# Kernel tuning notes

Hardware: AMD Instinct MI355X
Metric: run time of the kernel (lower is better)

Reference implementation:

```python
import jax, jax.numpy as jnp
import numpy as np

N_NODES = 50000
N_EDGES = 800000
IN_CH = 256
H1, D1 = 4, 64   # layer 1: 4 heads x 64 -> 256
H2, D2 = 1, 64   # output layer: 1 head x 64
NEG_SLOPE = 0.2  # DGL GATConv default


def _leaky_relu(x):
    return jnp.where(x >= 0, x, NEG_SLOPE * x)


def gat_conv(h, src, dst, W, attn_l, attn_r, bias, res_W, num_heads, out_feats, apply_elu):
    """DGL GATConv (eval mode, feat_drop=attn_drop=0).
    h: (N, F_in); src/dst: (E,) edge endpoints (edge u->v aggregates at v).
    W: (F_in, H*D); attn_l/attn_r: (H, D); bias: (H*D,); res_W: (F_in, H*D) or None.
    Returns (N, H, D).
    """
    N = h.shape[0]
    ft = (h @ W).reshape(N, num_heads, out_feats)            # (N,H,D)
    el = jnp.sum(ft * attn_l, axis=-1)                        # (N,H)
    er = jnp.sum(ft * attn_r, axis=-1)                        # (N,H)
    e = _leaky_relu(el[src] + er[dst])                        # (E,H)
    # segment softmax over incoming edges of each dst node
    emax = jax.ops.segment_max(e, dst, num_segments=N)        # (N,H)
    emax = jax.lax.stop_gradient(emax)
    ee = jnp.exp(e - emax[dst])                               # (E,H)
    denom = jax.ops.segment_sum(ee, dst, num_segments=N)      # (N,H)
    a = ee / denom[dst]                                       # (E,H)
    msg = ft[src] * a[:, :, None]                             # (E,H,D)
    rst = jax.ops.segment_sum(msg, dst, num_segments=N)       # (N,H,D)
    if res_W is not None:
        rst = rst + (h @ res_W).reshape(N, num_heads, out_feats)
    rst = rst + bias.reshape(num_heads, out_feats)
    if apply_elu:
        rst = jax.nn.elu(rst)
    return rst


def setup_inputs() -> dict:
    key = jax.random.key(0)
    ks = jax.random.split(key, 12)
    feat = jax.random.normal(ks[0], (N_NODES, IN_CH), dtype=jnp.float32)
    src = jax.random.randint(ks[1], (N_EDGES,), 0, N_NODES)
    dst = jax.random.randint(ks[2], (N_EDGES,), 0, N_NODES)
    s = 0.1
    W1 = jax.random.normal(ks[3], (IN_CH, H1 * D1), dtype=jnp.float32) * s
    al1 = jax.random.normal(ks[4], (H1, D1), dtype=jnp.float32) * s
    ar1 = jax.random.normal(ks[5], (H1, D1), dtype=jnp.float32) * s
    b1 = jnp.zeros((H1 * D1,), dtype=jnp.float32)
    W2 = jax.random.normal(ks[6], (H1 * D1, H2 * D2), dtype=jnp.float32) * s
    al2 = jax.random.normal(ks[7], (H2, D2), dtype=jnp.float32) * s
    ar2 = jax.random.normal(ks[8], (H2, D2), dtype=jnp.float32) * s
    b2 = jnp.zeros((H2 * D2,), dtype=jnp.float32)
    resW2 = jax.random.normal(ks[9], (H1 * D1, H2 * D2), dtype=jnp.float32) * s
    return {"feat": feat, "src": src, "dst": dst,
            "W1": W1, "al1": al1, "ar1": ar1, "b1": b1,
            "W2": W2, "al2": al2, "ar2": ar2, "b2": b2, "resW2": resW2}


def reference(feat, src, dst, W1, al1, ar1, b1, W2, al2, ar2, b2, resW2):
    # Layer 1: 4 heads, ELU, no residual (first DGL layer built without residual)
    h = gat_conv(feat, src, dst, W1, al1, ar1, b1, None, H1, D1, True)
    h = h.reshape(N_NODES, H1 * D1)  # flatten(1)
    # Layer 2: 1 head, residual (linear res_fc since 256 != 64), no activation
    h = gat_conv(h, src, dst, W2, al2, ar2, b2, resW2, H2, D2, False)
    return h.mean(axis=1)  # mean over output heads -> (N, out_channels)
```

## Files before the change

### kernel.cpp

```cpp
#include <hip/hip_runtime.h>
#include <math.h>

#define N_NODES 50000
#define N_EDGES 800000
#define ELL_W 64

#define NB 98
#define BCAP 10240
#define BIN_BLKS 250
#define CONV_BLKS 256

typedef __attribute__((ext_vector_type(8))) short bf16x8;
typedef __attribute__((ext_vector_type(4))) float f32x4;
typedef __attribute__((ext_vector_type(2))) float f32x2;

__device__ __forceinline__ float leaky(float x) { return x >= 0.f ? x : 0.2f * x; }
__device__ __forceinline__ unsigned short f2bf(float f) {
  unsigned u = __float_as_uint(f);
  return (unsigned short)((u + 0x7fffu + ((u >> 16) & 1u)) >> 16);
}
__device__ __forceinline__ float bflo(unsigned u) { return __uint_as_float(u << 16); }
__device__ __forceinline__ float bfhi(unsigned u) { return __uint_as_float(u & 0xffff0000u); }
__device__ __forceinline__ unsigned pack2(float a, float b) {
  return (unsigned)f2bf(a) | ((unsigned)f2bf(b) << 16);
}
__device__ __forceinline__ unsigned pack2u(unsigned a, unsigned b) {
  return pack2(__uint_as_float(a), __uint_as_float(b));
}

__launch_bounds__(256)
__global__ void prep_k(const float* __restrict__ W1, const float* __restrict__ W2,
                       const float* __restrict__ resW2, short* __restrict__ Wt1,
                       short* __restrict__ Wt2, const int* __restrict__ src,
                       const int* __restrict__ dst, unsigned* __restrict__ gcnt,
                       unsigned* __restrict__ bbuf) {
  __shared__ int hist[NB];
  __shared__ int basev[NB];
  if (blockIdx.x < BIN_BLKS) {
    const int e0 = blockIdx.x * (N_EDGES / BIN_BLKS);
    for (int i = threadIdx.x; i < NB; i += 256) hist[i] = 0;
    __syncthreads();
    for (int i = threadIdx.x; i < N_EDGES / BIN_BLKS; i += 256)
      atomicAdd(&hist[dst[e0 + i] >> 9], 1);
    __syncthreads();
    for (int b = threadIdx.x; b < NB; b += 256)
      basev[b] = (int)atomicAdd(&gcnt[b], (unsigned)hist[b]);
    __syncthreads();
    for (int i = threadIdx.x; i < NB; i += 256) hist[i] = 0;
    __syncthreads();
    for (int i = threadIdx.x; i < N_EDGES / BIN_BLKS; i += 256) {
      int d = dst[e0 + i], s = src[e0 + i];
      int b = d >> 9;
      int ofs = atomicAdd(&hist[b], 1);
      bbuf[(size_t)b * BCAP + basev[b] + ofs] =
          (unsigned)s | ((unsigned)(d & 511) << 16);
    }
    return;
  }
  const int gtid = (blockIdx.x - BIN_BLKS) * 256 + threadIdx.x;
  const int gsz = CONV_BLKS * 256;
  for (int idx = gtid; idx < 256 * 256; idx += gsz) {
    int n = idx >> 8, k = idx & 255;
    Wt1[idx] = (short)f2bf(W1[(size_t)k * 256 + n]);
  }
  for (int idx = gtid; idx < 128 * 256; idx += gsz) {
    int n = idx >> 8, k = idx & 255;
    float v = (n < 64) ? W2[(size_t)k * 64 + n] : resW2[(size_t)k * 64 + (n - 64)];
    Wt2[idx] = (short)f2bf(v);
  }
}

template <int MODE, bool SCAT>
__launch_bounds__(256)
__global__ void mfma_gemm_k(const short* __restrict__ A, const float* __restrict__ Af,
                            const short* __restrict__ Bt,
                            const float* __restrict__ bias, const float* __restrict__ al,
                            const float* __restrict__ ar, float* __restrict__ elp,
                            float* __restrict__ erp, short* __restrict__ Cb,
                            float* __restrict__ Cf, const unsigned* __restrict__ gcnt,
                            const unsigned* __restrict__ bbuf, int* __restrict__ cnt,
                            unsigned short* __restrict__ ell, int M, int K, int N) {
  constexpr int EPI_COLS = (MODE == 0) ? 136 : 72;
  union SharedU {
    struct { short As[4][128][8]; short Bs[4][128][8]; } ab;
    short epi[128 * EPI_COLS];
    int fill_cnt[512];
  };
  __shared__ SharedU sh;

  if (SCAT && blockIdx.y == 0) {
    if (blockIdx.x >= NB) return;
    const int b = blockIdx.x;
    int* cl = sh.fill_cnt;
    for (int i = threadIdx.x; i < 512; i += 256) cl[i] = 0;
    __syncthreads();
    const int n = min((int)gcnt[b], BCAP);
    const unsigned* bp = bbuf + (size_t)b * BCAP;
    for (int i = threadIdx.x; i < n; i += 256) {
      unsigned e = bp[i];
      int dl = (int)(e >> 16), s = (int)(e & 0xFFFFu);
      int sl = atomicAdd(&cl[dl], 1);
      if (sl < ELL_W)
        ell[((size_t)(b << 9) + dl) * ELL_W + sl] = (unsigned short)s;
    }
    __syncthreads();
    const int base = b << 9;
    for (int i = threadIdx.x; i < 512; i += 256) {
      int node = base + i;
      if (node < N_NODES) cnt[node] = cl[i];
    }
    return;
  }
  const int tid = threadIdx.x;
  const int bm0 = blockIdx.x * 128;
  const int bn0 = (SCAT ? ((int)blockIdx.y - 1) : (int)blockIdx.y) * 128;
  const int wave = tid >> 6, lane = tid & 63;
  const int wm = (wave & 1) * 64, wn = (wave >> 1) * 64;
  const int q = lane >> 4, r16 = lane & 15;
  const int srow = tid >> 1, sk = (tid & 1) * 16, sq = (tid & 1) * 2;
  f32x4 acc[4][4] = {};

  for (int k0 = 0; k0 < K; k0 += 32) {
    if (MODE == 0) {
      uint4 w0 = {0, 0, 0, 0}, w1 = {0, 0, 0, 0}, w2 = {0, 0, 0, 0}, w3 = {0, 0, 0, 0};
      if (bm0 + srow < M) {
        const uint4* p = (const uint4*)(Af + (size_t)(bm0 + srow) * K + k0 + sk);
        w0 = p[0];
        w1 = p[1];
        w2 = p[2];
        w3 = p[3];
      }
      uint4 v0, v1;
      v0.x = pack2u(w0.x, w0.y);
      v0.y = pack2u(w0.z, w0.w);
      v0.z = pack2u(w1.x, w1.y);
      v0.w = pack2u(w1.z, w1.w);
      v1.x = pack2u(w2.x, w2.y);
      v1.y = pack2u(w2.z, w2.w);
      v1.z = pack2u(w3.x, w3.y);
      v1.w = pack2u(w3.z, w3.w);
      *(uint4*)&sh.ab.As[sq][srow][0] = v0;
      *(uint4*)&sh.ab.As[sq + 1][srow][0] = v1;
    } else {
      uint4 v0 = {0, 0, 0, 0}, v1 = {0, 0, 0, 0};
      if (bm0 + srow < M) {
        const uint4* p = (const uint4*)(A + (size_t)(bm0 + srow) * K + k0 + sk);
        v0 = p[0];
        v1 = p[1];
      }
      *(uint4*)&sh.ab.As[sq][srow][0] = v0;
      *(uint4*)&sh.ab.As[sq + 1][srow][0] = v1;
    }
    {
      const uint4* p = (const uint4*)(Bt + (size_t)(bn0 + srow) * K + k0 + sk);
      *(uint4*)&sh.ab.Bs[sq][srow][0] = p[0];
      *(uint4*)&sh.ab.Bs[sq + 1][srow][0] = p[1];
    }
    __syncthreads();
    bf16x8 af[4], bfr[4];
#pragma unroll
    for (int i = 0; i < 4; ++i) af[i] = *(const bf16x8*)&sh.ab.As[q][wm + i * 16 + r16][0];
#pragma unroll
    for (int j = 0; j < 4; ++j) bfr[j] = *(const bf16x8*)&sh.ab.Bs[q][wn + j * 16 + r16][0];
#pragma unroll
    for (int i = 0; i < 4; ++i)
#pragma unroll
      for (int j = 0; j < 4; ++j)
        acc[i][j] = __builtin_amdgcn_mfma_f32_16x16x32_bf16(af[i], bfr[j], acc[i][j], 0, 0, 0);
    __syncthreads();
  }

  if (MODE == 0 || wn == 0) {
    const int head = (bn0 + wn) >> 6;
    float alv[4], arv[4];
#pragma unroll
    for (int j = 0; j < 4; ++j) {
      alv[j] = al[((MODE == 0) ? head * 64 : 0) + j * 16 + r16];
      arv[j] = ar[((MODE == 0) ? head * 64 : 0) + j * 16 + r16];
    }
#pragma unroll
    for (int i = 0; i < 4; ++i) {
#pragma unroll
      for (int reg = 0; reg < 4; ++reg) {
        float dl = acc[i][0][reg] * alv[0] + acc[i][1][reg] * alv[1] +
                   acc[i][2][reg] * alv[2] + acc[i][3][reg] * alv[3];
        float dr = acc[i][0][reg] * arv[0] + acc[i][1][reg] * arv[1] +
                   acc[i][2][reg] * arv[2] + acc[i][3][reg] * arv[3];
#pragma unroll
        for (int mm = 1; mm < 16; mm <<= 1) {
          dl += __shfl_xor(dl, mm);
          dr += __shfl_xor(dr, mm);
        }
        int row_g = bm0 + wm + i * 16 + q * 4 + reg;
        if (r16 == 0 && row_g < M) {
          if (MODE == 0) {
            elp[(size_t)row_g * 4 + head] = dl;
            erp[(size_t)row_g * 4 + head] = dr;
          } else {
            elp[row_g] = dl;
            erp[row_g] = dr;
          }
        }
      }
    }
  }

  if (MODE == 0) {
#pragma unroll
    for (int i = 0; i < 4; ++i)
#pragma unroll
      for (int reg = 0; reg < 4; ++reg) {
        int row = wm + i * 16 + q * 4 + reg;
#pragma unroll
        for (int j = 0; j < 4; ++j)
          sh.epi[row * EPI_COLS + wn + j * 16 + r16] = (short)f2bf(acc[i][j][reg]);
      }
    __syncthreads();
#pragma unroll
    for (int k = 0; k < 8; ++k) {
      int c = k * 256 + tid;
      int row = c >> 4, cc = c & 15;
      int row_g = bm0 + row;
      if (row_g < M) {
        uint4 v = *(const uint4*)&sh.epi[row * EPI_COLS + cc * 8];
        *(uint4*)(Cb + (size_t)row_g * N + bn0 + cc * 8) = v;
      }
    }
  } else {
    if (wn == 0) {
#pragma unroll
      for (int i = 0; i < 4; ++i)
#pragma unroll
        for (int reg = 0; reg < 4; ++reg) {
          int row = wm + i * 16 + q * 4 + reg;
#pragma unroll
          for (int j = 0; j < 4; ++j)
            sh.epi[row * EPI_COLS + j * 16 + r16] = (short)f2bf(acc[i][j][reg]);
        }
    } else {
#pragma unroll
      for (int i = 0; i < 4; ++i)
#pragma unroll
        for (int reg = 0; reg < 4; ++reg) {
          int row_g = bm0 + wm + i * 16 + q * 4 + reg;
          if (row_g >= M) continue;
#pragma unroll
          for (int j = 0; j < 4; ++j) {
            int col = j * 16 + r16;
            Cf[(size_t)row_g * 64 + col] = acc[i][j][reg] + bias[col];
          }
        }
    }
    __syncthreads();
#pragma unroll
    for (int k = 0; k < 4; ++k) {
      int c = k * 256 + tid;
      int row = c >> 3, cc = c & 7;
      int row_g = bm0 + row;
      if (row_g < M) {
        uint4 v = *(const uint4*)&sh.epi[row * EPI_COLS + cc * 8];
        *(uint4*)(Cb + (size_t)row_g * 64 + cc * 8) = v;
      }
    }
  }
}

#define AGG1_FMA(ACC, U, W)                     \
  {                                             \
    f32x2 w2_ = {(W), (W)};                     \
    ACC[0] += w2_ * (f32x2){bflo((U).x), bfhi((U).x)}; \
    ACC[1] += w2_ * (f32x2){bflo((U).y), bfhi((U).y)}; \
    ACC[2] += w2_ * (f32x2){bflo((U).z), bfhi((U).z)}; \
    ACC[3] += w2_ * (f32x2){bflo((U).w), bfhi((U).w)}; \
  }

__launch_bounds__(256)
__global__ void agg1_k(const unsigned short* __restrict__ ell, const int* __restrict__ cnt,
                       const float* __restrict__ el, const float* __restrict__ er,
                       const short* __restrict__ ft, const float* __restrict__ bias,
                       short* __restrict__ h1) {
  __shared__ uint2 wmeta[4][2][64][4];
  const int wv = threadIdx.x >> 6;
  const int lane = threadIdx.x & 63;
  const int nodeA = blockIdx.x * 8 + wv * 2;
  const int nodeB = nodeA + 1;
  const int degA = min(cnt[nodeA], ELL_W);
  const int degB = min(cnt[nodeB], ELL_W);
  const unsigned short* rowA = ell + nodeA * ELL_W;
  const unsigned short* rowB = ell + nodeB * ELL_W;

  {
    int sA = lane < degA ? (int)rowA[lane] : (degA > 0 ? (int)rowA[0] : 0);
    int sB = lane < degB ? (int)rowB[lane] : (degB > 0 ? (int)rowB[0] : 0);
    float4 elA = *(const float4*)(el + (size_t)sA * 4);
    float4 elB = *(const float4*)(el + (size_t)sB * 4);
    float4 erA = *(const float4*)(er + (size_t)nodeA * 4);
    float4 erB = *(const float4*)(er + (size_t)nodeB * 4);
    float a0 = lane < degA ? __expf(leaky(elA.x + erA.x)) : 0.f;
    float a1 = lane < degA ? __expf(leaky(elA.y + erA.y)) : 0.f;
    float a2 = lane < degA ? __expf(leaky(elA.z + erA.z)) : 0.f;
    float a3 = lane < degA ? __expf(leaky(elA.w + erA.w)) : 0.f;
    float b0 = lane < degB ? __expf(leaky(elB.x + erB.x)) : 0.f;
    float b1 = lane < degB ? __expf(leaky(elB.y + erB.y)) : 0.f;
    float b2 = lane < degB ? __expf(leaky(elB.z + erB.z)) : 0.f;
    float b3 = lane < degB ? __expf(leaky(elB.w + erB.w)) : 0.f;
    float dA0 = a0, dA1 = a1, dA2 = a2, dA3 = a3;
    float dB0 = b0, dB1 = b1, dB2 = b2, dB3 = b3;
#pragma unroll
    for (int m = 1; m < 64; m <<= 1) {
      dA0 += __shfl_xor(dA0, m);
      dB0 += __shfl_xor(dB0, m);
      dA1 += __shfl_xor(dA1, m);
      dB1 += __shfl_xor(dB1, m);
      dA2 += __shfl_xor(dA2, m);
      dB2 += __shfl_xor(dB2, m);
      dA3 += __shfl_xor(dA3, m);
      dB3 += __shfl_xor(dB3, m);
    }
    unsigned ofA = (unsigned)sA * 512u, ofB = (unsigned)sB * 512u;
    uint4 pa0, pa1, pb0, pb1;
    pa0.x = ofA; pa0.y = __float_as_uint(degA > 0 ? a0 / dA0 : 0.f);
    pa0.z = ofA; pa0.w = __float_as_uint(degA > 0 ? a1 / dA1 : 0.f);
    pa1.x = ofA; pa1.y = __float_as_uint(degA > 0 ? a2 / dA2 : 0.f);
    pa1.z = ofA; pa1.w = __float_as_uint(degA > 0 ? a3 / dA3 : 0.f);
    pb0.x = ofB; pb0.y = __float_as_uint(degB > 0 ? b0 / dB0 : 0.f);
    pb0.z = ofB; pb0.w = __float_as_uint(degB > 0 ? b1 / dB1 : 0.f);
    pb1.x = ofB; pb1.y = __float_as_uint(degB > 0 ? b2 / dB2 : 0.f);
    pb1.z = ofB; pb1.w = __float_as_uint(degB > 0 ? b3 / dB3 : 0.f);
    *(uint4*)&wmeta[wv][0][lane][0] = pa0;
    *(uint4*)&wmeta[wv][0][lane][2] = pa1;
    *(uint4*)&wmeta[wv][1][lane][0] = pb0;
    *(uint4*)&wmeta[wv][1][lane][2] = pb1;
  }

  const int half = lane >> 5, l5 = lane & 31, h = l5 >> 3;
  const char* ftb = (const char*)ft + l5 * 16;
  f32x2 accA[4] = {}, accB[4] = {};
  const int degM = max((degA + 7) & ~7, (degB + 7) & ~7);
  for (int i = 0; i < degM; i += 8) {
    unsigned oA[4], oB[4];
    float wA[4], wB[4];
#pragma unroll
    for (int k = 0; k < 4; ++k) {
      uint2 mA = wmeta[wv][0][i + k * 2 + half][h];
      uint2 mB = wmeta[wv][1][i + k * 2 + half][h];
      oA[k] = mA.x;
      wA[k] = __uint_as_float(mA.y);
      oB[k] = mB.x;
      wB[k] = __uint_as_float(mB.y);
    }
    uint4 uA[4], uB[4];
#pragma unroll
    for (int k = 0; k < 4; ++k) {
      uA[k] = *(const uint4*)(ftb + oA[k]);
      uB[k] = *(const uint4*)(ftb + oB[k]);
    }
#pragma unroll
    for (int k = 0; k < 4; ++k) {
      AGG1_FMA(accA, uA[k], wA[k]);
      AGG1_FMA(accB, uB[k], wB[k]);
    }
  }

#pragma unroll
  for (int j = 0; j < 4; ++j) {
    accA[j][0] += __shfl_xor(accA[j][0], 32);
    accA[j][1] += __shfl_xor(accA[j][1], 32);
    accB[j][0] += __shfl_xor(accB[j][0], 32);
    accB[j][1] += __shfl_xor(accB[j][1], 32);
  }
  const int node = half ? nodeB : nodeA;
  float v[8];
#pragma unroll
  for (int j = 0; j < 4; ++j) {
    v[2 * j] = half ? accB[j][0] : accA[j][0];
    v[2 * j + 1] = half ? accB[j][1] : accA[j][1];
  }
  float4 b0 = *(const float4*)(bias + l5 * 8);
  float4 b1 = *(const float4*)(bias + l5 * 8 + 4);
  v[0] += b0.x; v[1] += b0.y; v[2] += b0.z; v[3] += b0.w;
  v[4] += b1.x; v[5] += b1.y; v[6] += b1.z; v[7] += b1.w;
#pragma unroll
  for (int k = 0; k < 8; ++k) v[k] = v[k] > 0.f ? v[k] : expm1f(v[k]);
  uint4 o;
  o.x = pack2(v[0], v[1]);
  o.y = pack2(v[2], v[3]);
  o.z = pack2(v[4], v[5]);
  o.w = pack2(v[6], v[7]);
  *(uint4*)(h1 + (size_t)node * 256 + l5 * 8) = o;
}

__launch_bounds__(256)
__global__ void agg2_k(const unsigned short* __restrict__ ell, const int* __restrict__ cnt,
                       const float* __restrict__ el, const float* __restrict__ er,
                       const short* __restrict__ ft, float* __restrict__ out) {
  __shared__ uint2 wsl[4][2][64];
  const int wv = threadIdx.x >> 6;
  const int lane = threadIdx.x & 63;
  const int nodeA = blockIdx.x * 8 + wv * 2;
  const int nodeB = nodeA + 1;
  const int degA = min(cnt[nodeA], ELL_W);
  const int degB = min(cnt[nodeB], ELL_W);
  const unsigned short* rowA = ell + nodeA * ELL_W;
  const unsigned short* rowB = ell + nodeB * ELL_W;

  {
    int sA = lane < degA ? (int)rowA[lane] : (degA > 0 ? (int)rowA[0] : 0);
    int sB = lane < degB ? (int)rowB[lane] : (degB > 0 ? (int)rowB[0] : 0);
    float wa = lane < degA ? __expf(leaky(el[sA] + er[nodeA])) : 0.f;
    float wb = lane < degB ? __expf(leaky(el[sB] + er[nodeB])) : 0.f;
    float da = wa, db = wb;
#pragma unroll
    for (int m = 1; m < 64; m <<= 1) {
      da += __shfl_xor(da, m);
      db += __shfl_xor(db, m);
    }
    uint2 ea, eb;
    ea.x = (unsigned)sA * 128u;
    ea.y = __float_as_uint(degA > 0 ? wa / da : 0.f);
    eb.x = (unsigned)sB * 128u;
    eb.y = __float_as_uint(degB > 0 ? wb / db : 0.f);
    wsl[wv][0][lane] = ea;
    wsl[wv][1][lane] = eb;
  }

  const int qtr = lane >> 4, l4 = lane & 15;
  const char* ftb = (const char*)ft + l4 * 8;
  f32x2 accA[2] = {}, accB[2] = {};
  const int degM = max((degA + 7) & ~7, (degB + 7) & ~7);
  for (int i = 0; i < degM; i += 8) {
#pragma unroll
    for (int k = 0; k < 2; ++k) {
      int slot = i + k * 4 + qtr;
      uint2 ea = wsl[wv][0][slot];
      uint2 eb = wsl[wv][1][slot];
      uint2 ua = *(const uint2*)(ftb + ea.x);
      uint2 ub = *(const uint2*)(ftb + eb.x);
      float wa = __uint_as_float(ea.y);
      float wb = __uint_as_float(eb.y);
      f32x2 wa2 = {wa, wa}, wb2 = {wb, wb};
      accA[0] += wa2 * (f32x2){bflo(ua.x), bfhi(ua.x)};
      accA[1] += wa2 * (f32x2){bflo(ua.y), bfhi(ua.y)};
      accB[0] += wb2 * (f32x2){bflo(ub.x), bfhi(ub.x)};
      accB[1] += wb2 * (f32x2){bflo(ub.y), bfhi(ub.y)};
    }
  }
#pragma unroll
  for (int j = 0; j < 2; ++j) {
#pragma unroll
    for (int c = 0; c < 2; ++c) {
      accA[j][c] += __shfl_xor(accA[j][c], 16);
      accA[j][c] += __shfl_xor(accA[j][c], 32);
      accB[j][c] += __shfl_xor(accB[j][c], 16);
      accB[j][c] += __shfl_xor(accB[j][c], 32);
    }
  }
  if (lane < 32) {
    const int node = lane < 16 ? nodeA : nodeB;
    float4 add;
    add.x = lane < 16 ? accA[0][0] : accB[0][0];
    add.y = lane < 16 ? accA[0][1] : accB[0][1];
    add.z = lane < 16 ? accA[1][0] : accB[1][0];
    add.w = lane < 16 ? accA[1][1] : accB[1][1];
    float4* po = (float4*)(out + (size_t)node * 64 + l4 * 4);
    float4 o = *po;
    o.x += add.x;
    o.y += add.y;
    o.z += add.z;
    o.w += add.w;
    *po = o;
  }
}

extern "C" void kernel_launch(void* const* d_in, const int* in_sizes, int n_in,
                              void* d_out, int out_size, void* d_ws, size_t ws_size,
                              hipStream_t stream) {
  const float* feat  = (const float*)d_in[0];
  const int*   src   = (const int*)d_in[1];
  const int*   dst   = (const int*)d_in[2];
  const float* W1    = (const float*)d_in[3];
  const float* al1   = (const float*)d_in[4];
  const float* ar1   = (const float*)d_in[5];
  const float* b1    = (const float*)d_in[6];
  const float* W2    = (const float*)d_in[7];
  const float* al2   = (const float*)d_in[8];
  const float* ar2   = (const float*)d_in[9];
  const float* b2    = (const float*)d_in[10];
  const float* resW2 = (const float*)d_in[11];
  float* out = (float*)d_out;

  char* p = (char*)d_ws;
  short* ft1b = (short*)p; p += (size_t)N_NODES * 256 * 2;
  short* h1b  = (short*)p; p += (size_t)N_NODES * 256 * 2;
  short* ft2b = (short*)p; p += (size_t)N_NODES * 64 * 2;
  short* Wt1  = (short*)p; p += 256 * 256 * 2;
  short* Wt2  = (short*)p; p += 128 * 256 * 2;
  float* el1  = (float*)p; p += (size_t)N_NODES * 4 * 4;
  float* er1  = (float*)p; p += (size_t)N_NODES * 4 * 4;
  float* el2  = (float*)p; p += (size_t)N_NODES * 4;
  float* er2  = (float*)p; p += (size_t)N_NODES * 4;
  int* cnt    = (int*)p;   p += (size_t)N_NODES * 4;
  unsigned short* ell = (unsigned short*)p; p += (size_t)N_NODES * ELL_W * 2;
  unsigned* gcnt = (unsigned*)p; p += 128 * 4;
  unsigned* bbuf = (unsigned*)p; p += (size_t)NB * BCAP * 4;

  hipMemsetAsync(gcnt, 0, 128 * sizeof(unsigned), stream);

  dim3 blk(256);

  prep_k<<<BIN_BLKS + CONV_BLKS, blk, 0, stream>>>(W1, W2, resW2, Wt1, Wt2,
                                                   src, dst, gcnt, bbuf);

  mfma_gemm_k<0, true><<<dim3(391, 3), blk, 0, stream>>>(
      nullptr, feat, Wt1, nullptr, al1, ar1, el1, er1, ft1b, nullptr,
      gcnt, bbuf, cnt, ell, N_NODES, 256, 256);
  agg1_k<<<6250, blk, 0, stream>>>(ell, cnt, el1, er1, ft1b, b1, h1b);

  mfma_gemm_k<1, false><<<dim3(391, 1), blk, 0, stream>>>(
      h1b, nullptr, Wt2, b2, al2, ar2, el2, er2, ft2b, out,
      nullptr, nullptr, nullptr, nullptr, N_NODES, 256, 128);
  agg2_k<<<6250, blk, 0, stream>>>(ell, cnt, el2, er2, ft2b, out);
}
```

Before: 262.4 us.

## Replace padded ELL adjacency with compact CSR built by per-bin counting sort

The scatter stage now histograms each destination bin, does a block-wide prefix scan, and counting-sorts the source indices into a compact CSR array, packing offset and capped degree into one word per node. The aggregation kernels read that packed word instead of separate count and fixed-width ELL rows. The aim is to shrink adjacency storage and memory traffic and to make neighbour lists contiguous. In exchange the scatter blocks do more work, including a serial loop over earlier bins' counts. The first aggregation is also split into two launches over node halves, which adds a launch for no clear gain.

```diff
diff --git a/kernel.cpp b/kernel.cpp
--- a/kernel.cpp
+++ b/kernel.cpp
@@ -3,7 +3,7 @@
 
 #define N_NODES 50000
 #define N_EDGES 800000
-#define ELL_W 64
+#define DEG_CAP 64
 
 #define NB 98
 #define BCAP 10240
@@ -78,37 +78,63 @@
                             const float* __restrict__ ar, float* __restrict__ elp,
                             float* __restrict__ erp, short* __restrict__ Cb,
                             float* __restrict__ Cf, const unsigned* __restrict__ gcnt,
-                            const unsigned* __restrict__ bbuf, int* __restrict__ cnt,
-                            unsigned short* __restrict__ ell, int M, int K, int N) {
+                            const unsigned* __restrict__ bbuf,
+                            unsigned* __restrict__ meta,
+                            unsigned short* __restrict__ csr, int M, int K, int N) {
   constexpr int EPI_COLS = (MODE == 0) ? 136 : 72;
   union SharedU {
     struct { short As[4][128][8]; short Bs[4][128][8]; } ab;
     short epi[128 * EPI_COLS];
-    int fill_cnt[512];
+    struct { int h[512]; int o[512]; unsigned short s[BCAP]; } p2;
   };
   __shared__ SharedU sh;
+  __shared__ int wsum[4];
 
   if (SCAT && blockIdx.y == 0) {
     if (blockIdx.x >= NB) return;
     const int b = blockIdx.x;
-    int* cl = sh.fill_cnt;
-    for (int i = threadIdx.x; i < 512; i += 256) cl[i] = 0;
-    __syncthreads();
-    const int n = min((int)gcnt[b], BCAP);
+    const int tid = threadIdx.x;
+    int* h = sh.p2.h;
+    int* o = sh.p2.o;
+    unsigned short* srt = sh.p2.s;
+    for (int i = tid; i < 512; i += 256) h[i] = 0;
+    __syncthreads();
+    const int nb = min((int)gcnt[b], BCAP);
     const unsigned* bp = bbuf + (size_t)b * BCAP;
-    for (int i = threadIdx.x; i < n; i += 256) {
+    for (int i = tid; i < nb; i += 256) atomicAdd(&h[bp[i] >> 16], 1);
+    __syncthreads();
+    const int lane = tid & 63, wvi = tid >> 6;
+    int h0 = h[tid * 2], h1 = h[tid * 2 + 1];
+    int s2 = h0 + h1;
+    int v = s2;
+#pragma unroll
+    for (int d = 1; d < 64; d <<= 1) {
+      int t = __shfl_up(v, d);
+      if (lane >= d) v += t;
+    }
+    if (lane == 63) wsum[wvi] = v;
+    __syncthreads();
+    int wexcl = 0;
+    for (int j = 0; j < wvi; ++j) wexcl += wsum[j];
+    int excl = wexcl + v - s2;
+    o[tid * 2] = excl;
+    o[tid * 2 + 1] = excl + h0;
+    __syncthreads();
+    int bbase = 0;
+    for (int j = 0; j < b; ++j) bbase += min((int)gcnt[j], BCAP);
+    for (int i = tid; i < 512; i += 256) {
+      int node = (b << 9) + i;
+      if (node < N_NODES)
+        meta[node] = (unsigned)(bbase + o[i]) | ((unsigned)min(h[i], DEG_CAP) << 25);
+    }
+    __syncthreads();
+    for (int i = tid; i < nb; i += 256) {
       unsigned e = bp[i];
-      int dl = (int)(e >> 16), s = (int)(e & 0xFFFFu);
-      int sl = atomicAdd(&cl[dl], 1);
-      if (sl < ELL_W)
-        ell[((size_t)(b << 9) + dl) * ELL_W + sl] = (unsigned short)s;
-    }
-    __syncthreads();
-    const int base = b << 9;
-    for (int i = threadIdx.x; i < 512; i += 256) {
-      int node = base + i;
-      if (node < N_NODES) cnt[node] = cl[i];
-    }
+      int pos = atomicAdd(&o[e >> 16], 1);
+      srt[pos] = (unsigned short)(e & 0xFFFFu);
+    }
+    __syncthreads();
+    for (int i = tid; i < nb; i += 256) csr[bbase + i] = srt[i];
     return;
   }
   const int tid = threadIdx.x;
@@ -275,19 +301,20 @@
   }
 
 __launch_bounds__(256)
-__global__ void agg1_k(const unsigned short* __restrict__ ell, const int* __restrict__ cnt,
+__global__ void agg1_k(const unsigned short* __restrict__ csr,
+                       const unsigned* __restrict__ meta,
                        const float* __restrict__ el, const float* __restrict__ er,
                        const short* __restrict__ ft, const float* __restrict__ bias,
-                       short* __restrict__ h1) {
+                       short* __restrict__ h1, int node0) {
   __shared__ uint2 wmeta[4][2][64][4];
   const int wv = threadIdx.x >> 6;
   const int lane = threadIdx.x & 63;
-  const int nodeA = blockIdx.x * 8 + wv * 2;
+  const int nodeA = node0 + blockIdx.x * 8 + wv * 2;
   const int nodeB = nodeA + 1;
-  const int degA = min(cnt[nodeA], ELL_W);
-  const int degB = min(cnt[nodeB], ELL_W);
-  const unsigned short* rowA = ell + nodeA * ELL_W;
-  const unsigned short* rowB = ell + nodeB * ELL_W;
+  const unsigned mA = meta[nodeA], mB = meta[nodeB];
+  const int degA = (int)(mA >> 25), degB = (int)(mB >> 25);
+  const unsigned short* rowA = csr + (mA & 0x1FFFFFFu);
+  const unsigned short* rowB = csr + (mB & 0x1FFFFFFu);
 
   {
     int sA = lane < degA ? (int)rowA[lane] : (degA > 0 ? (int)rowA[0] : 0);
@@ -342,12 +369,12 @@
     float wA[4], wB[4];
 #pragma unroll
     for (int k = 0; k < 4; ++k) {
-      uint2 mA = wmeta[wv][0][i + k * 2 + half][h];
-      uint2 mB = wmeta[wv][1][i + k * 2 + half][h];
-      oA[k] = mA.x;
-      wA[k] = __uint_as_float(mA.y);
-      oB[k] = mB.x;
-      wB[k] = __uint_as_float(mB.y);
+      uint2 mAx = wmeta[wv][0][i + k * 2 + half][h];
+      uint2 mBx = wmeta[wv][1][i + k * 2 + half][h];
+      oA[k] = mAx.x;
+      wA[k] = __uint_as_float(mAx.y);
+      oB[k] = mBx.x;
+      wB[k] = __uint_as_float(mBx.y);
     }
     uint4 uA[4], uB[4];
 #pragma unroll
@@ -391,7 +418,8 @@
 }
 
 __launch_bounds__(256)
-__global__ void agg2_k(const unsigned short* __restrict__ ell, const int* __restrict__ cnt,
+__global__ void agg2_k(const unsigned short* __restrict__ csr,
+                       const unsigned* __restrict__ meta,
                        const float* __restrict__ el, const float* __restrict__ er,
                        const short* __restrict__ ft, float* __restrict__ out) {
   __shared__ uint2 wsl[4][2][64];
@@ -399,10 +427,10 @@
   const int lane = threadIdx.x & 63;
   const int nodeA = blockIdx.x * 8 + wv * 2;
   const int nodeB = nodeA + 1;
-  const int degA = min(cnt[nodeA], ELL_W);
-  const int degB = min(cnt[nodeB], ELL_W);
-  const unsigned short* rowA = ell + nodeA * ELL_W;
-  const unsigned short* rowB = ell + nodeB * ELL_W;
+  const unsigned mA = meta[nodeA], mB = meta[nodeB];
+  const int degA = (int)(mA >> 25), degB = (int)(mB >> 25);
+  const unsigned short* rowA = csr + (mA & 0x1FFFFFFu);
+  const unsigned short* rowB = csr + (mB & 0x1FFFFFFu);
 
   {
     int sA = lane < degA ? (int)rowA[lane] : (degA > 0 ? (int)rowA[0] : 0);
@@ -499,8 +527,8 @@
   float* er1  = (float*)p; p += (size_t)N_NODES * 4 * 4;
   float* el2  = (float*)p; p += (size_t)N_NODES * 4;
   float* er2  = (float*)p; p += (size_t)N_NODES * 4;
-  int* cnt    = (int*)p;   p += (size_t)N_NODES * 4;
-  unsigned short* ell = (unsigned short*)p; p += (size_t)N_NODES * ELL_W * 2;
+  unsigned* meta = (unsigned*)p; p += (size_t)N_NODES * 4;
+  unsigned short* csr = (unsigned short*)p; p += ((size_t)N_EDGES + 64) * 2;
   unsigned* gcnt = (unsigned*)p; p += 128 * 4;
   unsigned* bbuf = (unsigned*)p; p += (size_t)NB * BCAP * 4;
 
@@ -513,11 +541,12 @@
 
   mfma_gemm_k<0, true><<<dim3(391, 3), blk, 0, stream>>>(
       nullptr, feat, Wt1, nullptr, al1, ar1, el1, er1, ft1b, nullptr,
-      gcnt, bbuf, cnt, ell, N_NODES, 256, 256);
-  agg1_k<<<6250, blk, 0, stream>>>(ell, cnt, el1, er1, ft1b, b1, h1b);
+      gcnt, bbuf, meta, csr, N_NODES, 256, 256);
+  agg1_k<<<3125, blk, 0, stream>>>(csr, meta, el1, er1, ft1b, b1, h1b, 0);
+  agg1_k<<<3125, blk, 0, stream>>>(csr, meta, el1, er1, ft1b, b1, h1b, 25000);
 
   mfma_gemm_k<1, false><<<dim3(391, 1), blk, 0, stream>>>(
       h1b, nullptr, Wt2, b2, al2, ar2, el2, er2, ft2b, out,
       nullptr, nullptr, nullptr, nullptr, N_NODES, 256, 128);
-  agg2_k<<<6250, blk, 0, stream>>>(ell, cnt, el2, er2, ft2b, out);
-}
+  agg2_k<<<6250, blk, 0, stream>>>(csr, meta, el2, er2, ft2b, out);
+}
```

Result: no change. 265.3 us (+1.1%).

## Use finer dst bins and build ELL rows in shared memory before coalesced store

Applied to the files above, without the earlier changes.

Edges are now binned into 392 buckets of 128 destination nodes instead of 98 buckets of 512, which gives more scatter blocks. Each scatter block builds its ELL slab in LDS and then writes it to global memory as coalesced 16-byte stores, replacing scattered 2-byte global writes. Degree clamping moves into the scatter stage, so the aggregation kernels read cnt directly. The trade-offs are a larger shared-memory footprint in the scatter path and a smaller per-bin capacity (2816 edges); edges past that capacity are now dropped.

```diff
diff --git a/kernel.cpp b/kernel.cpp
--- a/kernel.cpp
+++ b/kernel.cpp
@@ -5,8 +5,8 @@
 #define N_EDGES 800000
 #define ELL_W 64
 
-#define NB 98
-#define BCAP 10240
+#define NB 392
+#define BCAP 2816
 #define BIN_BLKS 250
 #define CONV_BLKS 256
 
@@ -41,7 +41,7 @@
     for (int i = threadIdx.x; i < NB; i += 256) hist[i] = 0;
     __syncthreads();
     for (int i = threadIdx.x; i < N_EDGES / BIN_BLKS; i += 256)
-      atomicAdd(&hist[dst[e0 + i] >> 9], 1);
+      atomicAdd(&hist[dst[e0 + i] >> 7], 1);
     __syncthreads();
     for (int b = threadIdx.x; b < NB; b += 256)
       basev[b] = (int)atomicAdd(&gcnt[b], (unsigned)hist[b]);
@@ -50,10 +50,11 @@
     __syncthreads();
     for (int i = threadIdx.x; i < N_EDGES / BIN_BLKS; i += 256) {
       int d = dst[e0 + i], s = src[e0 + i];
-      int b = d >> 9;
+      int b = d >> 7;
       int ofs = atomicAdd(&hist[b], 1);
-      bbuf[(size_t)b * BCAP + basev[b] + ofs] =
-          (unsigned)s | ((unsigned)(d & 511) << 16);
+      int pos = basev[b] + ofs;
+      if (pos < BCAP)
+        bbuf[(size_t)b * BCAP + pos] = (unsigned)s | ((unsigned)(d & 127) << 16);
     }
     return;
   }
@@ -84,30 +85,37 @@
   union SharedU {
     struct { short As[4][128][8]; short Bs[4][128][8]; } ab;
     short epi[128 * EPI_COLS];
-    int fill_cnt[512];
+    struct { int h[128]; unsigned short lell[128 * ELL_W]; } p2;
   };
   __shared__ SharedU sh;
 
   if (SCAT && blockIdx.y == 0) {
     if (blockIdx.x >= NB) return;
     const int b = blockIdx.x;
-    int* cl = sh.fill_cnt;
-    for (int i = threadIdx.x; i < 512; i += 256) cl[i] = 0;
-    __syncthreads();
-    const int n = min((int)gcnt[b], BCAP);
+    const int tid = threadIdx.x;
+    int* h = sh.p2.h;
+    unsigned short* lell = sh.p2.lell;
+    for (int i = tid; i < 128; i += 256) h[i] = 0;
+    __syncthreads();
+    const int nb = min((int)gcnt[b], BCAP);
     const unsigned* bp = bbuf + (size_t)b * BCAP;
-    for (int i = threadIdx.x; i < n; i += 256) {
+    for (int i = tid; i < nb; i += 256) {
       unsigned e = bp[i];
-      int dl = (int)(e >> 16), s = (int)(e & 0xFFFFu);
-      int sl = atomicAdd(&cl[dl], 1);
-      if (sl < ELL_W)
-        ell[((size_t)(b << 9) + dl) * ELL_W + sl] = (unsigned short)s;
-    }
-    __syncthreads();
-    const int base = b << 9;
-    for (int i = threadIdx.x; i < 512; i += 256) {
+      int dl = (int)(e >> 16);
+      int sl = atomicAdd(&h[dl], 1);
+      if (sl < ELL_W) lell[dl * ELL_W + sl] = (unsigned short)(e & 0xFFFFu);
+    }
+    __syncthreads();
+    {
+      const uint4* ls = (const uint4*)lell;
+      uint4* gd = (uint4*)(ell + (size_t)b * 128 * ELL_W);
+#pragma unroll
+      for (int k = 0; k < 4; ++k) gd[k * 256 + tid] = ls[k * 256 + tid];
+    }
+    const int base = b << 7;
+    for (int i = tid; i < 128; i += 256) {
       int node = base + i;
-      if (node < N_NODES) cnt[node] = cl[i];
+      if (node < N_NODES) cnt[node] = min(h[i], ELL_W);
     }
     return;
   }
@@ -284,10 +292,10 @@
   const int lane = threadIdx.x & 63;
   const int nodeA = blockIdx.x * 8 + wv * 2;
   const int nodeB = nodeA + 1;
-  const int degA = min(cnt[nodeA], ELL_W);
-  const int degB = min(cnt[nodeB], ELL_W);
-  const unsigned short* rowA = ell + nodeA * ELL_W;
-  const unsigned short* rowB = ell + nodeB * ELL_W;
+  const int degA = cnt[nodeA];
+  const int degB = cnt[nodeB];
+  const unsigned short* rowA = ell + (size_t)nodeA * ELL_W;
+  const unsigned short* rowB = ell + (size_t)nodeB * ELL_W;
 
   {
     int sA = lane < degA ? (int)rowA[lane] : (degA > 0 ? (int)rowA[0] : 0);
@@ -399,10 +407,10 @@
   const int lane = threadIdx.x & 63;
   const int nodeA = blockIdx.x * 8 + wv * 2;
   const int nodeB = nodeA + 1;
-  const int degA = min(cnt[nodeA], ELL_W);
-  const int degB = min(cnt[nodeB], ELL_W);
-  const unsigned short* rowA = ell + nodeA * ELL_W;
-  const unsigned short* rowB = ell + nodeB * ELL_W;
+  const int degA = cnt[nodeA];
+  const int degB = cnt[nodeB];
+  const unsigned short* rowA = ell + (size_t)nodeA * ELL_W;
+  const unsigned short* rowB = ell + (size_t)nodeB * ELL_W;
 
   {
     int sA = lane < degA ? (int)rowA[lane] : (degA > 0 ? (int)rowA[0] : 0);
@@ -500,18 +508,18 @@
   float* el2  = (float*)p; p += (size_t)N_NODES * 4;
   float* er2  = (float*)p; p += (size_t)N_NODES * 4;
   int* cnt    = (int*)p;   p += (size_t)N_NODES * 4;
-  unsigned short* ell = (unsigned short*)p; p += (size_t)N_NODES * ELL_W * 2;
-  unsigned* gcnt = (unsigned*)p; p += 128 * 4;
+  unsigned short* ell = (unsigned short*)p; p += (size_t)NB * 128 * ELL_W * 2;
+  unsigned* gcnt = (unsigned*)p; p += 512 * 4;
   unsigned* bbuf = (unsigned*)p; p += (size_t)NB * BCAP * 4;
 
-  hipMemsetAsync(gcnt, 0, 128 * sizeof(unsigned), stream);
+  hipMemsetAsync(gcnt, 0, 512 * sizeof(unsigned), stream);
 
   dim3 blk(256);
 
   prep_k<<<BIN_BLKS + CONV_BLKS, blk, 0, stream>>>(W1, W2, resW2, Wt1, Wt2,
                                                    src, dst, gcnt, bbuf);
 
-  mfma_gemm_k<0, true><<<dim3(391, 3), blk, 0, stream>>>(
+  mfma_gemm_k<0, true><<<dim3(392, 3), blk, 0, stream>>>(
       nullptr, feat, Wt1, nullptr, al1, ar1, el1, er1, ft1b, nullptr,
       gcnt, bbuf, cnt, ell, N_NODES, 256, 256);
   agg1_k<<<6250, blk, 0, stream>>>(ell, cnt, el1, er1, ft1b, b1, h1b);
```

Result: no change. 262.3 us (-0.0%).
